# Kernel tuning notes

Hardware: AMD Instinct MI355X
Metric: run time of the kernel (lower is better)

## Reference

```python
import jax, jax.numpy as jnp
import numpy as np

HEAD_SIZE = 16  # matches init_kwargs head_size


def _rope_angles(seq_len, half_dim, base=10000.0):
    # standard RoPE frequencies, matches typical precompute_pos_cis
    freqs = 1.0 / (base ** (np.arange(0, half_dim, dtype=np.float32) / half_dim))
    t = np.arange(seq_len, dtype=np.float32)
    ang = np.outer(t, freqs)  # (S, half_dim)
    return jnp.asarray(np.cos(ang)), jnp.asarray(np.sin(ang))


def setup_inputs() -> dict:
    key = jax.random.key(0)
    ks = jax.random.split(key, 10)
    B, S, D = 2, 2048, 1024
    hd = D // HEAD_SIZE
    pos_cos, pos_sin = _rope_angles(S, hd // 2)
    w = lambda k: jax.random.normal(k, (D, D), jnp.float32) * 0.02
    b = lambda k: jax.random.normal(k, (D,), jnp.float32) * 0.02
    return {
        "x": jax.random.normal(ks[0], (B, S, D), jnp.float32),
        "pos_cos": pos_cos,
        "pos_sin": pos_sin,
        "wq_w": w(ks[1]), "wq_b": b(ks[2]),
        "wk_w": w(ks[3]), "wk_b": b(ks[4]),
        "wv_w": w(ks[5]), "wv_b": b(ks[6]),
        "wo_w": w(ks[7]), "wo_b": b(ks[8]),
    }


def _apply_rope(t, cos, sin):
    # t: (B, S, H, hd); cos/sin: (S, hd//2) -> broadcast (1, S, 1, hd//2)
    B, S, H, hd = t.shape
    tr = t.reshape(B, S, H, hd // 2, 2)
    a, b = tr[..., 0], tr[..., 1]
    c = cos[None, :, None, :]
    s = sin[None, :, None, :]
    # complex multiply (a + ib) * (c + is)
    out_r = a * c - b * s
    out_i = a * s + b * c
    return jnp.stack([out_r, out_i], axis=-1).reshape(B, S, H, hd)


def reference(x, pos_cos, pos_sin, wq_w, wq_b, wk_w, wk_b, wv_w, wv_b, wo_w, wo_b):
    B, S, D = x.shape
    H = HEAD_SIZE
    hd = D // H
    q = (x @ wq_w.T + wq_b).reshape(B, S, H, hd)
    k = (x @ wk_w.T + wk_b).reshape(B, S, H, hd)
    v = (x @ wv_w.T + wv_b).reshape(B, S, H, hd)
    q = _apply_rope(q, pos_cos, pos_sin)
    k = _apply_rope(k, pos_cos, pos_sin)
    scale = 1.0 / jnp.sqrt(jnp.asarray(hd, x.dtype))
    scores = jnp.einsum('bshd,bthd->bhst', q, k) * scale  # (B,H,S,S)
    causal = jnp.tril(jnp.ones((S, S), bool))
    scores = jnp.where(causal[None, None], scores, jnp.asarray(-jnp.inf, scores.dtype))
    probs = jax.nn.softmax(scores, axis=-1)
    out = jnp.einsum('bhst,bthd->bshd', probs, v).reshape(B, S, D)
    return out @ wo_w.T + wo_b
```

## Files before the change

kernel.cpp:

```cpp
#include <hip/hip_runtime.h>
#include <stdint.h>
#include <stddef.h>


typedef __bf16 bf16x8 __attribute__((ext_vector_type(8)));
typedef float  f32x4  __attribute__((ext_vector_type(4)));

__device__ __forceinline__ unsigned short f2b(float f) {
  union { float f; uint32_t u; } v; v.f = f;
  uint32_t u = v.u;
  return (unsigned short)((u + 0x7FFFu + ((u >> 16) & 1u)) >> 16);
}

__device__ __forceinline__ uint32_t cvtpk(float lo, float hi) {
  uint32_t r;
  asm("v_cvt_pk_bf16_f32 %0, %1, %2" : "=v"(r) : "v"(lo), "v"(hi));
  return r;
}

__global__ void cast_all_kernel(const float* __restrict__ x,
                                const float* __restrict__ wq,
                                const float* __restrict__ wk,
                                const float* __restrict__ wv,
                                const float* __restrict__ wo,
                                unsigned short* __restrict__ xbf,
                                unsigned short* __restrict__ wqkv,
                                unsigned short* __restrict__ wobf) {
  int i = blockIdx.x * blockDim.x + threadIdx.x;
  const float* src;
  unsigned short* dst;
  int rem;
  if (i < 524288) {
    src = x; dst = xbf; rem = i;
  } else if (i < 917504) {
    rem = i - 524288;
    const int mat = rem >> 17;
    src = (mat == 0) ? wq : (mat == 1) ? wk : wv;
    dst = wqkv;
  } else {
    rem = i - 917504;
    src = wo; dst = wobf;
  }
  const int inmat = (i < 524288) ? rem : (i < 917504) ? (rem & 131071) : rem;
  const int L  = inmat & 1023;
  const int kt = (inmat >> 10) & 15;
  const int pn = inmat >> 14;
  const int row = pn * 128 + ((L >> 7) << 4) + (L & 15);
  const int k0  = kt * 64 + ((L >> 4) & 7) * 8;
  const float4* s = (const float4*)(src + (size_t)row * 1024 + k0);
  float4 a = s[0], b = s[1];
  uint4 pk;
  pk.x = (uint32_t)f2b(a.x) | ((uint32_t)f2b(a.y) << 16);
  pk.y = (uint32_t)f2b(a.z) | ((uint32_t)f2b(a.w) << 16);
  pk.z = (uint32_t)f2b(b.x) | ((uint32_t)f2b(b.y) << 16);
  pk.w = (uint32_t)f2b(b.z) | ((uint32_t)f2b(b.w) << 16);
  *(uint4*)(dst + (size_t)rem * 8) = pk;
}

__global__ __launch_bounds__(256, 3) void qkv_gemm_kernel(
    const unsigned short* __restrict__ A,
    const unsigned short* __restrict__ W,
    const float* __restrict__ biasq, const float* __restrict__ biask,
    const float* __restrict__ biasv,
    const float* __restrict__ cp, const float* __restrict__ sp,
    unsigned short* __restrict__ qo,
    unsigned short* __restrict__ ko,
    unsigned short* __restrict__ vo)
{
  const int tid  = threadIdx.x;
  const int w    = tid >> 6, l = tid & 63;
  const int lm   = l & 15,  quad = l >> 4;
  const int bid  = blockIdx.x;
  const int xcd  = bid & 7, slot = bid >> 3;
  const int by   = (xcd >> 1) * 8 + slot / 12;
  const int nblk = (xcd & 1) * 12 + slot % 12;
  const int m0   = by * 128;
  const int wm   = (w >> 1) * 64, wn = (w & 1) * 64;

  const unsigned short* At = A + (size_t)by * 16 * 8192;
  const unsigned short* Wt = W + (size_t)nblk * 16 * 8192;

  const f32x4 fzero = {0.f, 0.f, 0.f, 0.f};
  f32x4 acc[4][4];
#pragma unroll
  for (int i = 0; i < 4; ++i)
#pragma unroll
    for (int j = 0; j < 4; ++j) acc[i][j] = fzero;

  bf16x8 pA[4], pB[4], qA[4], qB[4];

#define QKV_LOADH(DA, DB, T, KK)                                              \
  {                                                                           \
    const unsigned short* Ab_ = At + (size_t)(T) * 8192;                      \
    const unsigned short* Wb_ = Wt + (size_t)(T) * 8192;                      \
    _Pragma("unroll")                                                         \
    for (int i = 0; i < 4; ++i)                                               \
      DA[i] = *(const bf16x8*)(Ab_ +                                          \
          (size_t)((((w >> 1) * 4 + i) * 128 + (KK) * 64 + l)) * 8);          \
    _Pragma("unroll")                                                         \
    for (int j = 0; j < 4; ++j)                                               \
      DB[j] = *(const bf16x8*)(Wb_ +                                          \
          (size_t)((((w & 1) * 4 + j) * 128 + (KK) * 64 + l)) * 8);           \
  }

#define QKV_MFMAH(SA, SB)                                                     \
  _Pragma("unroll")                                                           \
  for (int i = 0; i < 4; ++i)                                                 \
    _Pragma("unroll")                                                         \
    for (int j = 0; j < 4; ++j)                                               \
      acc[i][j] = __builtin_amdgcn_mfma_f32_16x16x32_bf16(SA[i], SB[j],       \
                                                          acc[i][j], 0, 0, 0);

  QKV_LOADH(pA, pB, 0, 0);
#pragma unroll 1
  for (int t = 0; t < 16; ++t) {
    QKV_LOADH(qA, qB, t, 1);
    QKV_MFMAH(pA, pB);
    if (t < 15) QKV_LOADH(pA, pB, t + 1, 0);
    QKV_MFMAH(qA, qB);
  }
#undef QKV_LOADH
#undef QKV_MFMAH

  const int which = nblk >> 3;
  const int n0    = (nblk & 7) * 128;
  const float* bias = (which == 0) ? biasq : (which == 1) ? biask : biasv;
#pragma unroll
  for (int i = 0; i < 4; ++i) {
#pragma unroll
    for (int j = 0; j < 4; ++j) {
      const int n = n0 + wn + j * 16 + lm;
      const float bval = bias[n];
      const int h = n >> 6, d = n & 63;
      float vals[4];
#pragma unroll
      for (int r = 0; r < 4; ++r) {
        const int m = m0 + wm + i * 16 + quad * 4 + r;
        const int srow = m & 2047;
        float val = acc[i][j][r] + bval;
        if (which != 2) {
          const float c  = cp[srow * 32 + (d >> 1)];
          const float sn = sp[srow * 32 + (d >> 1)];
          const float part = __shfl_xor(val, 1, 64);
          val = (d & 1) ? (part * sn + val * c) : (val * c - part * sn);
        }
        vals[r] = val;
      }
      const int mbase = m0 + wm + i * 16 + quad * 4;
      const int b = mbase >> 11, s0 = mbase & 2047;
      const int bh = (b << 4) + h;
      if (which == 0) {
#pragma unroll
        for (int r = 0; r < 4; ++r)
          qo[((size_t)bh * 2048 + s0 + r) * 64 + d] = f2b(vals[r]);
      } else if (which == 1) {
#pragma unroll
        for (int r = 0; r < 4; ++r) {
          const int s = s0 + r;
          ko[((size_t)bh * 32 + (s >> 6)) * 4096 +
             (size_t)(((d >> 3) * 64 + (s & 63))) * 8 + (d & 7)] = f2b(vals[r]);
        }
      } else {
        uint32_t w0 = (uint32_t)f2b(vals[0]) | ((uint32_t)f2b(vals[1]) << 16);
        uint32_t w1 = (uint32_t)f2b(vals[2]) | ((uint32_t)f2b(vals[3]) << 16);
        uint2 pk; pk.x = w0; pk.y = w1;
        *(uint2*)(vo + ((size_t)bh * 32 + (s0 >> 6)) * 4096 +
                  (size_t)((((s0 & 63) >> 3) * 64 + d)) * 8 + (s0 & 7)) = pk;
      }
    }
  }
}

__global__ __launch_bounds__(256, 4) void flash_kernel(
    const unsigned short* __restrict__ Q,
    const unsigned short* __restrict__ K,
    const unsigned short* __restrict__ VT,
    unsigned short* __restrict__ O)
{
  constexpr int PSTRIDE = 72;
  constexpr float SC  = 0.18033688011f;
  constexpr float THR = 11.5416f;
  __shared__ unsigned short Ps[64 * PSTRIDE];
  const int tid = threadIdx.x;
  const int w = tid >> 6, l = tid & 63, lm = l & 15, quad = l >> 4;
  const int bh = blockIdx.x, qt = 31 - (int)blockIdx.y;
  const int row0 = qt * 64 + w * 16;

  bf16x8 aq[2];
#pragma unroll
  for (int kc = 0; kc < 2; ++kc)
    aq[kc] = *(const bf16x8*)(Q + ((size_t)bh * 2048 + row0 + lm) * 64 + kc * 32 + quad * 8);

  const f32x4 fzero = {0.f, 0.f, 0.f, 0.f};
  f32x4 Oacc[4];
#pragma unroll
  for (int jo = 0; jo < 4; ++jo) Oacc[jo] = fzero;
  float m_i = -1e30f, l_i = 0.f;

  const int nkv = qt + 1;

#pragma unroll 1
  for (int kt = 0; kt < nkv - 1; ++kt) {
    const size_t tbase = ((size_t)bh * 32 + kt) * 4096;
    bf16x8 kf[2][4], vf[2][4];
#pragma unroll
    for (int kc = 0; kc < 2; ++kc)
#pragma unroll
      for (int tb = 0; tb < 4; ++tb) {
        const size_t off = tbase + (size_t)(((kc * 4 + quad) * 64 + tb * 16 + lm)) * 8;
        kf[kc][tb] = *(const bf16x8*)(K + off);
        vf[kc][tb] = *(const bf16x8*)(VT + off);
      }
    f32x4 Sc[4];
#pragma unroll
    for (int tb = 0; tb < 4; ++tb) Sc[tb] = fzero;
#pragma unroll
    for (int kc = 0; kc < 2; ++kc)
#pragma unroll
      for (int tb = 0; tb < 4; ++tb)
        Sc[tb] = __builtin_amdgcn_mfma_f32_16x16x32_bf16(kf[kc][tb], aq[kc], Sc[tb], 0, 0, 0);

    float mx = -1e30f;
#pragma unroll
    for (int tb = 0; tb < 4; ++tb)
#pragma unroll
      for (int r = 0; r < 4; ++r) {
        float s = Sc[tb][r] * SC;
        Sc[tb][r] = s;
        mx = fmaxf(mx, s);
      }
    mx = fmaxf(mx, __shfl_xor(mx, 16, 64));
    mx = fmaxf(mx, __shfl_xor(mx, 32, 64));

    const bool skip = (bool)__all(mx - m_i <= THR);
    float alpha = 1.f;
    if (!skip) {
      const float mnew = fmaxf(m_i, mx);
      alpha = exp2f(m_i - mnew);
      m_i = mnew;
    }
    const float mref = m_i;

    float ps = 0.f;
#pragma unroll
    for (int tb = 0; tb < 4; ++tb) {
      float p0 = exp2f(Sc[tb][0] - mref), p1 = exp2f(Sc[tb][1] - mref);
      float p2 = exp2f(Sc[tb][2] - mref), p3 = exp2f(Sc[tb][3] - mref);
      ps += (p0 + p1) + (p2 + p3);
      uint2 pk;
      pk.x = cvtpk(p0, p1);
      pk.y = cvtpk(p2, p3);
      *(uint2*)(Ps + (size_t)(w * 16 + lm) * PSTRIDE + tb * 16 + quad * 4) = pk;
    }
    ps += __shfl_xor(ps, 16, 64);
    ps += __shfl_xor(ps, 32, 64);
    if (skip) {
      l_i += ps;
    } else {
      l_i = l_i * alpha + ps;
      float af4[4];
#pragma unroll
      for (int r = 0; r < 4; ++r) af4[r] = __shfl(alpha, quad * 4 + r, 64);
#pragma unroll
      for (int jo = 0; jo < 4; ++jo)
#pragma unroll
        for (int r = 0; r < 4; ++r) Oacc[jo][r] *= af4[r];
    }

#pragma unroll
    for (int kc = 0; kc < 2; ++kc) {
      bf16x8 ap = *(const bf16x8*)(Ps + (size_t)(w * 16 + lm) * PSTRIDE + kc * 32 + quad * 8);
#pragma unroll
      for (int jo = 0; jo < 4; ++jo)
        Oacc[jo] = __builtin_amdgcn_mfma_f32_16x16x32_bf16(ap, vf[kc][jo], Oacc[jo], 0, 0, 0);
    }
  }

  {
    const size_t tbase = ((size_t)bh * 32 + qt) * 4096;
    bf16x8 kf[2][4], vf[2][4];
#pragma unroll
    for (int kc = 0; kc < 2; ++kc)
#pragma unroll
      for (int tb = 0; tb < 4; ++tb) {
        const size_t off = tbase + (size_t)(((kc * 4 + quad) * 64 + tb * 16 + lm)) * 8;
        kf[kc][tb] = *(const bf16x8*)(K + off);
        vf[kc][tb] = *(const bf16x8*)(VT + off);
      }
    f32x4 Sc[4];
#pragma unroll
    for (int tb = 0; tb < 4; ++tb) Sc[tb] = fzero;
#pragma unroll
    for (int kc = 0; kc < 2; ++kc)
#pragma unroll
      for (int tb = 0; tb < 4; ++tb)
        Sc[tb] = __builtin_amdgcn_mfma_f32_16x16x32_bf16(kf[kc][tb], aq[kc], Sc[tb], 0, 0, 0);

    const int mrel = w * 16 + lm;
    float mx = -1e30f;
#pragma unroll
    for (int tb = 0; tb < 4; ++tb)
#pragma unroll
      for (int r = 0; r < 4; ++r) {
        float s = Sc[tb][r] * SC;
        if (tb * 16 + quad * 4 + r > mrel) s = -1e30f;
        Sc[tb][r] = s;
        mx = fmaxf(mx, s);
      }
    mx = fmaxf(mx, __shfl_xor(mx, 16, 64));
    mx = fmaxf(mx, __shfl_xor(mx, 32, 64));
    const float mnew  = fmaxf(m_i, mx);
    const float alpha = exp2f(m_i - mnew);
    m_i = mnew;

    float ps = 0.f;
#pragma unroll
    for (int tb = 0; tb < 4; ++tb) {
      float p0 = exp2f(Sc[tb][0] - mnew), p1 = exp2f(Sc[tb][1] - mnew);
      float p2 = exp2f(Sc[tb][2] - mnew), p3 = exp2f(Sc[tb][3] - mnew);
      ps += (p0 + p1) + (p2 + p3);
      uint2 pk;
      pk.x = cvtpk(p0, p1);
      pk.y = cvtpk(p2, p3);
      *(uint2*)(Ps + (size_t)(w * 16 + lm) * PSTRIDE + tb * 16 + quad * 4) = pk;
    }
    ps += __shfl_xor(ps, 16, 64);
    ps += __shfl_xor(ps, 32, 64);
    l_i = l_i * alpha + ps;

    float af4[4];
#pragma unroll
    for (int r = 0; r < 4; ++r) af4[r] = __shfl(alpha, quad * 4 + r, 64);
#pragma unroll
    for (int jo = 0; jo < 4; ++jo)
#pragma unroll
      for (int r = 0; r < 4; ++r) Oacc[jo][r] *= af4[r];

#pragma unroll
    for (int kc = 0; kc < 2; ++kc) {
      bf16x8 ap = *(const bf16x8*)(Ps + (size_t)(w * 16 + lm) * PSTRIDE + kc * 32 + quad * 8);
#pragma unroll
      for (int jo = 0; jo < 4; ++jo)
        Oacc[jo] = __builtin_amdgcn_mfma_f32_16x16x32_bf16(ap, vf[kc][jo], Oacc[jo], 0, 0, 0);
    }
  }

  float lf[4];
#pragma unroll
  for (int r = 0; r < 4; ++r) lf[r] = 1.0f / __shfl(l_i, quad * 4 + r, 64);
  const int b = bh >> 4, h = bh & 15;
  const size_t obase = ((size_t)((b * 16 + (qt >> 1)) * 16 + h)) * 8192;
  const int Lbase = ((qt & 1) * 4 + w) * 128 + quad * 4;
#pragma unroll
  for (int jo = 0; jo < 4; ++jo) {
    const int Ljo = Lbase + (jo * 2 + (lm >> 3)) * 16;
#pragma unroll
    for (int r = 0; r < 4; ++r)
      O[obase + (size_t)(Ljo + r) * 8 + (lm & 7)] = f2b(Oacc[jo][r] * lf[r]);
  }
}

__global__ __launch_bounds__(256, 2) void oproj_gemm_kernel(
    const unsigned short* __restrict__ A,
    const unsigned short* __restrict__ W,
    const float* __restrict__ bias,
    float* __restrict__ out)
{
  const int tid = threadIdx.x;
  const int w = tid >> 6, l = tid & 63;
  const int lm = l & 15, quad = l >> 4;
  const int nblk = blockIdx.x;
  const int m0 = blockIdx.y * 64;
  const int half = blockIdx.y & 1;

  const unsigned short* At = A + (size_t)(blockIdx.y >> 1) * 16 * 8192;
  const unsigned short* Wt = W + (size_t)nblk * 16 * 8192;

  const f32x4 fzero = {0.f, 0.f, 0.f, 0.f};
  f32x4 acc[4][2];
#pragma unroll
  for (int i = 0; i < 4; ++i)
#pragma unroll
    for (int j = 0; j < 2; ++j) acc[i][j] = fzero;

  bf16x8 pA[4], pB[2], qA[4], qB[2];

#define OP_LOADH(DA, DB, T, KK)                                               \
  {                                                                           \
    const unsigned short* Ab_ = At + (size_t)(T) * 8192;                      \
    const unsigned short* Wb_ = Wt + (size_t)(T) * 8192;                      \
    _Pragma("unroll")                                                         \
    for (int i = 0; i < 4; ++i)                                               \
      DA[i] = *(const bf16x8*)(Ab_ +                                          \
          (size_t)(((half * 4 + i) * 128 + (KK) * 64 + l)) * 8);              \
    _Pragma("unroll")                                                         \
    for (int j = 0; j < 2; ++j)                                               \
      DB[j] = *(const bf16x8*)(Wb_ +                                          \
          (size_t)(((w * 2 + j) * 128 + (KK) * 64 + l)) * 8);                 \
  }

#define OP_MFMAH(SA, SB)                                                      \
  _Pragma("unroll")                                                           \
  for (int i = 0; i < 4; ++i)                                                 \
    _Pragma("unroll")                                                         \
    for (int j = 0; j < 2; ++j)                                               \
      acc[i][j] = __builtin_amdgcn_mfma_f32_16x16x32_bf16(SA[i], SB[j],       \
                                                          acc[i][j], 0, 0, 0);

  OP_LOADH(pA, pB, 0, 0);
#pragma unroll 1
  for (int t = 0; t < 16; ++t) {
    OP_LOADH(qA, qB, t, 1);
    OP_MFMAH(pA, pB);
    if (t < 15) OP_LOADH(pA, pB, t + 1, 0);
    OP_MFMAH(qA, qB);
  }
#undef OP_LOADH
#undef OP_MFMAH

#pragma unroll
  for (int i = 0; i < 4; ++i) {
#pragma unroll
    for (int j = 0; j < 2; ++j) {
      const int n = nblk * 128 + w * 32 + j * 16 + lm;
      const float bval = bias[n];
#pragma unroll
      for (int r = 0; r < 4; ++r) {
        const int m = m0 + i * 16 + quad * 4 + r;
        out[(size_t)m * 1024 + n] = acc[i][j][r] + bval;
      }
    }
  }
}

extern "C" void kernel_launch(void* const* d_in, const int* in_sizes, int n_in,
                              void* d_out, int out_size, void* d_ws, size_t ws_size,
                              hipStream_t stream) {
  (void)in_sizes; (void)n_in; (void)out_size; (void)ws_size;
  const float* x  = (const float*)d_in[0];
  const float* cp = (const float*)d_in[1];
  const float* sp = (const float*)d_in[2];
  const float* wq = (const float*)d_in[3];
  const float* bq = (const float*)d_in[4];
  const float* wk = (const float*)d_in[5];
  const float* bk = (const float*)d_in[6];
  const float* wv = (const float*)d_in[7];
  const float* bv = (const float*)d_in[8];
  const float* wo = (const float*)d_in[9];
  const float* bo = (const float*)d_in[10];
  float* out = (float*)d_out;

  unsigned short* xbf  = (unsigned short*)d_ws;
  unsigned short* wqkv = xbf  + (size_t)4 * 1024 * 1024;
  unsigned short* wobf = wqkv + (size_t)3 * 1024 * 1024;
  unsigned short* qbf  = wobf + (size_t)1 * 1024 * 1024;
  unsigned short* kbf  = qbf  + (size_t)4 * 1024 * 1024;
  unsigned short* vbf  = kbf  + (size_t)4 * 1024 * 1024;
  unsigned short* obf  = vbf  + (size_t)4 * 1024 * 1024;

  hipLaunchKernelGGL(cast_all_kernel, dim3(4096), dim3(256), 0, stream,
                     x, wq, wk, wv, wo, xbf, wqkv, wobf);

  hipLaunchKernelGGL(qkv_gemm_kernel, dim3(768), dim3(256), 0, stream,
                     xbf, wqkv, bq, bk, bv, cp, sp, qbf, kbf, vbf);
  hipLaunchKernelGGL(flash_kernel, dim3(32, 32), dim3(256), 0, stream,
                     qbf, kbf, vbf, obf);
  hipLaunchKernelGGL(oproj_gemm_kernel, dim3(8, 64), dim3(256), 0, stream,
                     obf, wobf, bo, out);
}
```

Before: 202.0 us.

## Fold softmax scale into Q projection and triple-buffer QKV GEMM loads

```diff
diff --git a/kernel.cpp b/kernel.cpp
--- a/kernel.cpp
+++ b/kernel.cpp
@@ -67,6 +67,7 @@
     unsigned short* __restrict__ ko,
     unsigned short* __restrict__ vo)
 {
+  constexpr float QSC = 0.18033688011f;
   const int tid  = threadIdx.x;
   const int w    = tid >> 6, l = tid & 63;
   const int lm   = l & 15,  quad = l >> 4;
@@ -87,20 +88,21 @@
 #pragma unroll
     for (int j = 0; j < 4; ++j) acc[i][j] = fzero;
 
-  bf16x8 pA[4], pB[4], qA[4], qB[4];
-
-#define QKV_LOADH(DA, DB, T, KK)                                              \
+  bf16x8 aS0[4], bS0[4], aS1[4], bS1[4], aS2[4], bS2[4];
+
+#define QKV_LOADH(DA, DB, H)                                                  \
   {                                                                           \
-    const unsigned short* Ab_ = At + (size_t)(T) * 8192;                      \
-    const unsigned short* Wb_ = Wt + (size_t)(T) * 8192;                      \
+    const int T_ = (H) >> 1, KK_ = (H) & 1;                                   \
+    const unsigned short* Ab_ = At + (size_t)T_ * 8192;                       \
+    const unsigned short* Wb_ = Wt + (size_t)T_ * 8192;                       \
     _Pragma("unroll")                                                         \
     for (int i = 0; i < 4; ++i)                                               \
       DA[i] = *(const bf16x8*)(Ab_ +                                          \
-          (size_t)((((w >> 1) * 4 + i) * 128 + (KK) * 64 + l)) * 8);          \
+          (size_t)((((w >> 1) * 4 + i) * 128 + KK_ * 64 + l)) * 8);           \
     _Pragma("unroll")                                                         \
     for (int j = 0; j < 4; ++j)                                               \
       DB[j] = *(const bf16x8*)(Wb_ +                                          \
-          (size_t)((((w & 1) * 4 + j) * 128 + (KK) * 64 + l)) * 8);           \
+          (size_t)((((w & 1) * 4 + j) * 128 + KK_ * 64 + l)) * 8);            \
   }
 
 #define QKV_MFMAH(SA, SB)                                                     \
@@ -111,14 +113,16 @@
       acc[i][j] = __builtin_amdgcn_mfma_f32_16x16x32_bf16(SA[i], SB[j],       \
                                                           acc[i][j], 0, 0, 0);
 
-  QKV_LOADH(pA, pB, 0, 0);
+  QKV_LOADH(aS0, bS0, 0);
+  QKV_LOADH(aS1, bS1, 1);
 #pragma unroll 1
-  for (int t = 0; t < 16; ++t) {
-    QKV_LOADH(qA, qB, t, 1);
-    QKV_MFMAH(pA, pB);
-    if (t < 15) QKV_LOADH(pA, pB, t + 1, 0);
-    QKV_MFMAH(qA, qB);
-  }
+  for (int h = 0; h < 30; h += 3) {
+    QKV_LOADH(aS2, bS2, h + 2); QKV_MFMAH(aS0, bS0);
+    QKV_LOADH(aS0, bS0, h + 3); QKV_MFMAH(aS1, bS1);
+    QKV_LOADH(aS1, bS1, h + 4); QKV_MFMAH(aS2, bS2);
+  }
+  QKV_MFMAH(aS0, bS0);
+  QKV_MFMAH(aS1, bS1);
 #undef QKV_LOADH
 #undef QKV_MFMAH
 
@@ -152,7 +156,7 @@
       if (which == 0) {
 #pragma unroll
         for (int r = 0; r < 4; ++r)
-          qo[((size_t)bh * 2048 + s0 + r) * 64 + d] = f2b(vals[r]);
+          qo[((size_t)bh * 2048 + s0 + r) * 64 + d] = f2b(vals[r] * QSC);
       } else if (which == 1) {
 #pragma unroll
         for (int r = 0; r < 4; ++r) {
@@ -178,7 +182,6 @@
     unsigned short* __restrict__ O)
 {
   constexpr int PSTRIDE = 72;
-  constexpr float SC  = 0.18033688011f;
   constexpr float THR = 11.5416f;
   __shared__ unsigned short Ps[64 * PSTRIDE];
   const int tid = threadIdx.x;
@@ -220,15 +223,17 @@
       for (int tb = 0; tb < 4; ++tb)
         Sc[tb] = __builtin_amdgcn_mfma_f32_16x16x32_bf16(kf[kc][tb], aq[kc], Sc[tb], 0, 0, 0);
 
-    float mx = -1e30f;
-#pragma unroll
-    for (int tb = 0; tb < 4; ++tb)
-#pragma unroll
-      for (int r = 0; r < 4; ++r) {
-        float s = Sc[tb][r] * SC;
-        Sc[tb][r] = s;
-        mx = fmaxf(mx, s);
-      }
+    float m01, m23, mtb;
+    float mx;
+    {
+      float t0 = fmaxf(fmaxf(Sc[0][0], Sc[0][1]), fmaxf(Sc[0][2], Sc[0][3]));
+      float t1 = fmaxf(fmaxf(Sc[1][0], Sc[1][1]), fmaxf(Sc[1][2], Sc[1][3]));
+      float t2 = fmaxf(fmaxf(Sc[2][0], Sc[2][1]), fmaxf(Sc[2][2], Sc[2][3]));
+      float t3 = fmaxf(fmaxf(Sc[3][0], Sc[3][1]), fmaxf(Sc[3][2], Sc[3][3]));
+      m01 = fmaxf(t0, t1); m23 = fmaxf(t2, t3);
+      mtb = fmaxf(m01, m23);
+      mx  = mtb;
+    }
     mx = fmaxf(mx, __shfl_xor(mx, 16, 64));
     mx = fmaxf(mx, __shfl_xor(mx, 32, 64));
 
@@ -302,7 +307,7 @@
     for (int tb = 0; tb < 4; ++tb)
 #pragma unroll
       for (int r = 0; r < 4; ++r) {
-        float s = Sc[tb][r] * SC;
+        float s = Sc[tb][r];
         if (tb * 16 + quad * 4 + r > mrel) s = -1e30f;
         Sc[tb][r] = s;
         mx = fmaxf(mx, s);
```

Result: no change. 200.1 us (-0.9%).
